# Optimization experiments

Measured on AMD Instinct MI355X. Metric: run time of the kernel, lower is better.

Reference implementation:

```python
import jax, jax.numpy as jnp
import numpy as np
from jax.ops import segment_sum

N_NODES = 100000


def gcn_conv(x, W, b, src, dst, num_nodes):
    # PyG GCNConv: h = x @ W; add self-loops; symmetric normalization; aggregate; + bias
    h = x @ W  # [N, out]
    # add self-loops
    loops = jnp.arange(num_nodes, dtype=src.dtype)
    src_sl = jnp.concatenate([src, loops])
    dst_sl = jnp.concatenate([dst, loops])
    # degree over destination (incl. self-loops), edge weight = 1
    deg = segment_sum(jnp.ones_like(src_sl, dtype=h.dtype), dst_sl, num_segments=num_nodes)
    dinv = jnp.where(deg > 0, jax.lax.rsqrt(deg), 0.0)
    norm = dinv[src_sl] * dinv[dst_sl]  # [E+N]
    msg = h[src_sl] * norm[:, None]      # gather + scale, [E+N, out]
    out = segment_sum(msg, dst_sl, num_segments=num_nodes)  # scatter-add
    return out + b


def setup_inputs() -> dict:
    key = jax.random.key(0)
    ks = jax.random.split(key, 5)
    N, F, C = N_NODES, 64, 10
    E = 1600000
    x = jax.random.normal(ks[0], (N, F), dtype=jnp.float32)
    edge_index = jax.random.randint(ks[1], (2, E), 0, N, dtype=jnp.int64)
    W1 = jax.random.normal(ks[2], (F, 128), dtype=jnp.float32) * (1.0 / np.sqrt(F))
    b1 = jnp.zeros((128,), dtype=jnp.float32)
    W2 = jax.random.normal(ks[3], (128, 16), dtype=jnp.float32) * (1.0 / np.sqrt(128))
    b2 = jnp.zeros((16,), dtype=jnp.float32)
    Wl = jax.random.normal(ks[4], (16, C), dtype=jnp.float32) * (1.0 / np.sqrt(16))
    bl = jnp.zeros((C,), dtype=jnp.float32)
    return {"x": x, "edge_index": edge_index, "W1": W1, "b1": b1,
            "W2": W2, "b2": b2, "Wl": Wl, "bl": bl}


def reference(x, edge_index, W1, b1, W2, b2, Wl, bl):
    src, dst = edge_index[0], edge_index[1]
    h = gcn_conv(x, W1, b1, src, dst, N_NODES)
    h = jax.nn.relu(h)
    h = gcn_conv(h, W2, b2, src, dst, N_NODES)
    h = jax.nn.relu(h)
    return h @ Wl + bl
```

## Files before the change

### kernel.cpp

```cpp
#include <hip/hip_runtime.h>
#include <hip/hip_fp16.h>


#define F_IN 64
#define H1DIM 128
#define H2DIM 16
#define C_OUT 10

#define NBK 1024
#define BSZ_LOG 7
#define BNODES 128
#define CAP 2816
#define SRC_BITS 17

typedef _Float16 f16x8 __attribute__((ext_vector_type(8)));
typedef _Float16 f16x4 __attribute__((ext_vector_type(4)));
typedef float f32x4 __attribute__((ext_vector_type(4)));

__global__ void init_cursors(int* __restrict__ cur) {
    int t = blockIdx.x * 256 + threadIdx.x;
    if (t < NBK) cur[t] = t * CAP;
}

__global__ __launch_bounds__(256) void bucket_scatter(
        const int* __restrict__ ei, int E, int N,
        int* __restrict__ cursor, unsigned* __restrict__ pairs) {
    __shared__ int cnt[NBK];
    __shared__ int base[NBK];
    for (int t = threadIdx.x; t < NBK; t += 256) cnt[t] = 0;
    __syncthreads();

    const int4* s4 = (const int4*)ei;
    const int4* d4 = (const int4*)(ei + E);
    int chunk4 = blockIdx.x * 1024;
    int s_[16], d_[16];
    int m = 0;
#pragma unroll
    for (int r = 0; r < 4; r++) {
        int i4 = chunk4 + r * 256 + threadIdx.x;
        if (i4 * 4 < E) {
            int4 sv = s4[i4], dv = d4[i4];
            int ss[4] = {sv.x, sv.y, sv.z, sv.w};
            int dd[4] = {dv.x, dv.y, dv.z, dv.w};
#pragma unroll
            for (int q = 0; q < 4; q++) {
                if ((unsigned)ss[q] < (unsigned)N && (unsigned)dd[q] < (unsigned)N) {
                    s_[m] = ss[q]; d_[m] = dd[q]; m++;
                }
            }
        }
    }
    for (int k = 0; k < m; k++) atomicAdd(&cnt[d_[k] >> BSZ_LOG], 1);
    __syncthreads();
    for (int t = threadIdx.x; t < NBK; t += 256) {
        int c = cnt[t];
        base[t] = c ? atomicAdd(&cursor[t], c) : 0;
        cnt[t] = 0;
    }
    __syncthreads();
    for (int k = 0; k < m; k++) {
        int b = d_[k] >> BSZ_LOG;
        int pos = base[b] + atomicAdd(&cnt[b], 1);
        if (pos < (b + 1) * CAP)
            pairs[pos] = ((unsigned)(d_[k] & (BNODES - 1)) << SRC_BITS) | (unsigned)s_[k];
    }
}

__global__ __launch_bounds__(256) void build_csr_convert(
        const unsigned* __restrict__ pairs, const int* __restrict__ cursor,
        const float* __restrict__ x, int N,
        float* __restrict__ dinv, int* __restrict__ row_beg,
        int* __restrict__ row_end, int* __restrict__ csr_src,
        __half2* __restrict__ xh2) {
    int b = blockIdx.x;
    int base_node = b << BSZ_LOG;
    int nn = min(BNODES, N - base_node);
    __shared__ int cnt[BNODES];
    __shared__ int sc[BNODES];
    __shared__ int cur[BNODES];
    __shared__ float sdi[BNODES];
    int tid = threadIdx.x;
    if (tid < BNODES) cnt[tid] = 0;
    __syncthreads();

    int pbeg = b * CAP;
    int pend = min(cursor[b], (b + 1) * CAP);
    for (int j = pbeg + tid; j < pend; j += 256)
        atomicAdd(&cnt[pairs[j] >> SRC_BITS], 1);
    __syncthreads();

    int v = (tid < BNODES) ? cnt[tid] : 0;
    if (tid < BNODES) sc[tid] = v;
    __syncthreads();
#pragma unroll
    for (int off = 1; off < BNODES; off <<= 1) {
        int t = (tid < BNODES && tid >= off) ? sc[tid - off] : 0;
        __syncthreads();
        if (tid < BNODES) sc[tid] += t;
        __syncthreads();
    }
    if (tid < nn) {
        int ro = pbeg + sc[tid] - v;
        row_beg[base_node + tid] = ro;
        row_end[base_node + tid] = ro + v;
        cur[tid] = ro;
        float di = rsqrtf((float)(v + 1));
        dinv[base_node + tid] = di;
        sdi[tid] = di;
    }
    __syncthreads();

    for (int j = pbeg + tid; j < pend; j += 256) {
        unsigned p = pairs[j];
        int dl = p >> SRC_BITS, s = p & ((1u << SRC_BITS) - 1);
        int pos = atomicAdd(&cur[dl], 1);
        csr_src[pos] = s;
    }

    const float2* x2 = (const float2*)x;
    int total = nn * 32;
    for (int t = tid; t < total; t += 256) {
        int nl = t >> 5, l = t & 31;
        float di = sdi[nl];
        long long idx = (long long)(base_node + nl) * 32 + l;
        float2 xv = x2[idx];
        xh2[idx] = __floats2half2_rn(xv.x * di, xv.y * di);
    }
}

__global__ __launch_bounds__(256) void gather1_h2(
        const f16x8* __restrict__ xh8, const float* __restrict__ dinv,
        const int* __restrict__ row_beg, const int* __restrict__ row_end,
        const int* __restrict__ csr_src, int N, f16x8* __restrict__ agg1h8) {
    int node = (blockIdx.x * 256 + threadIdx.x) >> 3;
    if (node >= N) return;
    int p = threadIdx.x & 7;
    int beg = row_beg[node], end = row_end[node];
    f16x8 self = xh8[(size_t)node * 8 + p];
    float acc[8];
#pragma unroll
    for (int q = 0; q < 8; q++) acc[q] = (float)self[q];
    int j = beg;
    for (; j + 4 <= end; j += 4) {
        int s0 = csr_src[j], s1 = csr_src[j + 1];
        int s2 = csr_src[j + 2], s3 = csr_src[j + 3];
        f16x8 v0 = xh8[(size_t)s0 * 8 + p];
        f16x8 v1 = xh8[(size_t)s1 * 8 + p];
        f16x8 v2 = xh8[(size_t)s2 * 8 + p];
        f16x8 v3 = xh8[(size_t)s3 * 8 + p];
#pragma unroll
        for (int q = 0; q < 8; q++)
            acc[q] += ((float)v0[q] + (float)v1[q]) + ((float)v2[q] + (float)v3[q]);
    }
    for (; j < end; ++j) {
        f16x8 v = xh8[(size_t)csr_src[j] * 8 + p];
#pragma unroll
        for (int q = 0; q < 8; q++) acc[q] += (float)v[q];
    }
    float di = dinv[node];
    f16x8 o;
#pragma unroll
    for (int q = 0; q < 8; q++) o[q] = (_Float16)(acc[q] * di);
    agg1h8[(size_t)node * 8 + p] = o;
}

__global__ __launch_bounds__(256) void pack_weights(
        const float* __restrict__ W1, const float* __restrict__ W2,
        f16x8* __restrict__ W1p, f16x8* __restrict__ W2p) {
    int s = blockIdx.x * 256 + threadIdx.x;
    if (s < 1024) {
        int frag = s >> 6, lane = s & 63;
        int tile = frag >> 1, kf = frag & 1;
        int c = lane & 15, g = lane >> 4;
        f16x8 v;
#pragma unroll
        for (int j = 0; j < 8; ++j)
            v[j] = (_Float16)W1[(kf * 32 + g * 8 + j) * H1DIM + tile * 16 + c];
        W1p[s] = v;
    } else if (s < 1024 + 256) {
        int s2 = s - 1024;
        int f = s2 >> 6, lane = s2 & 63;
        int c = lane & 15, g = lane >> 4;
        f16x8 v;
#pragma unroll
        for (int j = 0; j < 8; ++j)
            v[j] = (_Float16)W2[(f * 32 + g * 8 + j) * H2DIM + c];
        W2p[s2] = v;
    }
}

__global__ __launch_bounds__(256) void dense1_mfma(
        const _Float16* __restrict__ agg, const f16x8* __restrict__ W1p,
        const f16x8* __restrict__ W2p, const float* __restrict__ b1,
        const float* __restrict__ dinv, int N, _Float16* __restrict__ z2h) {
    __shared__ float sb1[H1DIM];
    __shared__ _Float16 Hl[4][16 * H1DIM];
    if (threadIdx.x < H1DIM) sb1[threadIdx.x] = b1[threadIdx.x];
    __syncthreads();
    const int wave = threadIdx.x >> 6, lane = threadIdx.x & 63;
    const int c = lane & 15, g = lane >> 4;
    const int nodeBase = blockIdx.x * 64 + wave * 16;

    int nld = nodeBase + c; if (nld > N - 1) nld = N - 1;
    const f16x8 a0 = *(const f16x8*)(agg + (size_t)nld * 64 + g * 8);
    const f16x8 a1 = *(const f16x8*)(agg + (size_t)nld * 64 + 32 + g * 8);

    _Float16* hl = Hl[wave];
    const f32x4 zero = {0.f, 0.f, 0.f, 0.f};
#pragma unroll
    for (int t = 0; t < 8; ++t) {
        f32x4 d = __builtin_amdgcn_mfma_f32_16x16x32_f16(W1p[(t * 2 + 1) * 64 + lane], a1, zero, 0, 0, 0);
        d = __builtin_amdgcn_mfma_f32_16x16x32_f16(W1p[(t * 2 + 0) * 64 + lane], a0, d, 0, 0, 0);
        f16x4 hv;
#pragma unroll
        for (int r = 0; r < 4; ++r)
            hv[r] = (_Float16)fmaxf(d[r] + sb1[t * 16 + g * 4 + r], 0.f);
        unsigned byte = ((unsigned)c * 256 + (unsigned)t * 32 + (unsigned)g * 8) ^ ((unsigned)(c & 7) << 4);
        *(f16x4*)((char*)hl + byte) = hv;
    }

    f32x4 acc = zero;
#pragma unroll
    for (int f = 0; f < 4; ++f) {
        unsigned byte = ((unsigned)c * 256 + (unsigned)f * 64 + (unsigned)g * 16) ^ ((unsigned)(c & 7) << 4);
        f16x8 a2 = *(const f16x8*)((char*)hl + byte);
        acc = __builtin_amdgcn_mfma_f32_16x16x32_f16(a2, W2p[f * 64 + lane], acc, 0, 0, 0);
    }
#pragma unroll
    for (int r = 0; r < 4; ++r) {
        int node = nodeBase + g * 4 + r;
        if (node < N) z2h[(size_t)node * 16 + c] = (_Float16)(acc[r] * dinv[node]);
    }
}

__global__ __launch_bounds__(256) void gather2_final_v2(
        const __half2* __restrict__ z2h, const float* __restrict__ dinv,
        const int* __restrict__ row_beg, const int* __restrict__ row_end,
        const int* __restrict__ csr_src,
        const float* __restrict__ b2, const float* __restrict__ Wl,
        const float* __restrict__ bl, int N, float* __restrict__ out) {
    __shared__ float sWl[H2DIM * C_OUT];
    __shared__ float sb2[H2DIM];
    __shared__ float sbl[C_OUT];
    __shared__ float hbuf[32][17];
    int tid = threadIdx.x;
    if (tid < H2DIM * C_OUT) sWl[tid] = Wl[tid];
    if (tid < H2DIM) sb2[tid] = b2[tid];
    if (tid < C_OUT) sbl[tid] = bl[tid];
    __syncthreads();

    int node = blockIdx.x * 32 + (tid >> 3);
    int p = tid & 7;
    int ln = tid >> 3;
    if (node < N) {
        int beg = row_beg[node], end = row_end[node];
        float2 sv = __half22float2(z2h[(size_t)node * 8 + p]);
        float ax = sv.x, ay = sv.y;
        int j = beg;
        for (; j + 4 <= end; j += 4) {
            int s0 = csr_src[j], s1 = csr_src[j + 1];
            int s2 = csr_src[j + 2], s3 = csr_src[j + 3];
            float2 v0 = __half22float2(z2h[(size_t)s0 * 8 + p]);
            float2 v1 = __half22float2(z2h[(size_t)s1 * 8 + p]);
            float2 v2 = __half22float2(z2h[(size_t)s2 * 8 + p]);
            float2 v3 = __half22float2(z2h[(size_t)s3 * 8 + p]);
            ax += (v0.x + v1.x) + (v2.x + v3.x);
            ay += (v0.y + v1.y) + (v2.y + v3.y);
        }
        for (; j < end; ++j) {
            float2 v = __half22float2(z2h[(size_t)csr_src[j] * 8 + p]);
            ax += v.x; ay += v.y;
        }
        float di = dinv[node];
        hbuf[ln][2 * p]     = fmaxf(ax * di + sb2[2 * p], 0.f);
        hbuf[ln][2 * p + 1] = fmaxf(ay * di + sb2[2 * p + 1], 0.f);
    }
    __syncthreads();
    if (node < N) {
        float o0 = sbl[p];
        float o1 = (p < 2) ? sbl[8 + p] : 0.f;
#pragma unroll
        for (int k = 0; k < H2DIM; k++) {
            float hk = hbuf[ln][k];
            o0 = fmaf(hk, sWl[k * C_OUT + p], o0);
            if (p < 2) o1 = fmaf(hk, sWl[k * C_OUT + 8 + p], o1);
        }
        out[(size_t)node * C_OUT + p] = o0;
        if (p < 2) out[(size_t)node * C_OUT + 8 + p] = o1;
    }
}

extern "C" void kernel_launch(void* const* d_in, const int* in_sizes, int n_in,
                              void* d_out, int out_size, void* d_ws, size_t ws_size,
                              hipStream_t stream) {
    const float* x  = (const float*)d_in[0];
    const int*   ei = (const int*)d_in[1];
    const float* W1 = (const float*)d_in[2];
    const float* b1 = (const float*)d_in[3];
    const float* W2 = (const float*)d_in[4];
    const float* b2 = (const float*)d_in[5];
    const float* Wl = (const float*)d_in[6];
    const float* bl = (const float*)d_in[7];
    float* out = (float*)d_out;

    const int N = in_sizes[0] / F_IN;
    const int E = in_sizes[1] / 2;

    size_t off = 0;
    auto carve = [&](size_t bytes) {
        void* p = (char*)d_ws + off;
        off += (bytes + 255) & ~(size_t)255;
        return p;
    };
    float*   dinv    = (float*)  carve((size_t)N * sizeof(float));
    int*     row_beg = (int*)    carve((size_t)N * sizeof(int));
    int*     row_end = (int*)    carve((size_t)N * sizeof(int));
    int*     csr_src = (int*)    carve((size_t)NBK * CAP * sizeof(int));
    __half2* xh2     = (__half2*)carve((size_t)N * 32 * sizeof(__half2));
    size_t agg_bytes = (size_t)N * 32 * sizeof(__half2);
    size_t pr_bytes  = (size_t)NBK * CAP * sizeof(unsigned);
    __half2* agg1h   = (__half2*)carve(agg_bytes > pr_bytes ? agg_bytes : pr_bytes);
    __half2* z2h     = (__half2*)carve((size_t)N * 8 * sizeof(__half2));
    int*     bcur    = (int*)    carve(NBK * sizeof(int));
    f16x8*   W1p     = (f16x8*)  carve(1024 * sizeof(f16x8));
    f16x8*   W2p     = (f16x8*)  carve(256 * sizeof(f16x8));
    unsigned* pairs = (unsigned*)agg1h;

    const int nbuckets_used = (N + BNODES - 1) >> BSZ_LOG;

    init_cursors<<<(NBK + 255) / 256, 256, 0, stream>>>(bcur);
    pack_weights<<<5, 256, 0, stream>>>(W1, W2, W1p, W2p);
    bucket_scatter<<<(E + 4095) / 4096, 256, 0, stream>>>(ei, E, N, bcur, pairs);
    build_csr_convert<<<nbuckets_used, 256, 0, stream>>>(
        pairs, bcur, x, N, dinv, row_beg, row_end, csr_src, xh2);

    gather1_h2<<<((size_t)N * 8 + 255) / 256, 256, 0, stream>>>(
        (const f16x8*)xh2, dinv, row_beg, row_end, csr_src, N, (f16x8*)agg1h);
    dense1_mfma<<<(N + 63) / 64, 256, 0, stream>>>(
        (const _Float16*)agg1h, W1p, W2p, b1, dinv, N, (_Float16*)z2h);
    gather2_final_v2<<<(N + 31) / 32, 256, 0, stream>>>(
        z2h, dinv, row_beg, row_end, csr_src, b2, Wl, bl, N, out);
}
```

Measured before the change: 114.4 us.

## Merge setup kernels, stage bucket pairs in LDS, unroll gathers by eight

Merges cursor initialization and weight packing into one setup kernel, removing a launch. The CSR build kernel now copies each bucket's pairs into shared memory once and reuses them for both the counting and placement passes, instead of reading global memory twice. Both gather kernels gain an 8-way unrolled edge loop to put more independent loads in flight. This raises register and LDS use (about 11 KB per block for the pairs buffer), which may reduce occupancy.

Result: faster. 111.4 us (-2.6%).

```diff
diff --git a/kernel.cpp b/kernel.cpp
--- a/kernel.cpp
+++ b/kernel.cpp
@@ -17,9 +17,33 @@
 typedef _Float16 f16x4 __attribute__((ext_vector_type(4)));
 typedef float f32x4 __attribute__((ext_vector_type(4)));
 
-__global__ void init_cursors(int* __restrict__ cur) {
-    int t = blockIdx.x * 256 + threadIdx.x;
-    if (t < NBK) cur[t] = t * CAP;
+__global__ __launch_bounds__(256) void setup_kernel(
+        const float* __restrict__ W1, const float* __restrict__ W2,
+        f16x8* __restrict__ W1p, f16x8* __restrict__ W2p,
+        int* __restrict__ cur) {
+    int s = blockIdx.x * 256 + threadIdx.x;
+    if (s < 1024) {
+        int frag = s >> 6, lane = s & 63;
+        int tile = frag >> 1, kf = frag & 1;
+        int c = lane & 15, g = lane >> 4;
+        f16x8 v;
+#pragma unroll
+        for (int j = 0; j < 8; ++j)
+            v[j] = (_Float16)W1[(kf * 32 + g * 8 + j) * H1DIM + tile * 16 + c];
+        W1p[s] = v;
+    } else if (s < 1024 + 256) {
+        int s2 = s - 1024;
+        int f = s2 >> 6, lane = s2 & 63;
+        int c = lane & 15, g = lane >> 4;
+        f16x8 v;
+#pragma unroll
+        for (int j = 0; j < 8; ++j)
+            v[j] = (_Float16)W2[(f * 32 + g * 8 + j) * H2DIM + c];
+        W2p[s2] = v;
+    } else {
+        int t = s - 1280;
+        if (t >= 0 && t < NBK) cur[t] = t * CAP;
+    }
 }
 
 __global__ __launch_bounds__(256) void bucket_scatter(
@@ -75,18 +99,22 @@
     int b = blockIdx.x;
     int base_node = b << BSZ_LOG;
     int nn = min(BNODES, N - base_node);
+    __shared__ unsigned lp[CAP];
     __shared__ int cnt[BNODES];
     __shared__ int sc[BNODES];
     __shared__ int cur[BNODES];
     __shared__ float sdi[BNODES];
     int tid = threadIdx.x;
     if (tid < BNODES) cnt[tid] = 0;
-    __syncthreads();
 
     int pbeg = b * CAP;
     int pend = min(cursor[b], (b + 1) * CAP);
-    for (int j = pbeg + tid; j < pend; j += 256)
-        atomicAdd(&cnt[pairs[j] >> SRC_BITS], 1);
+    int np = pend - pbeg;
+    for (int j = tid; j < np; j += 256) lp[j] = pairs[pbeg + j];
+    __syncthreads();
+
+    for (int j = tid; j < np; j += 256)
+        atomicAdd(&cnt[lp[j] >> SRC_BITS], 1);
     __syncthreads();
 
     int v = (tid < BNODES) ? cnt[tid] : 0;
@@ -110,8 +138,8 @@
     }
     __syncthreads();
 
-    for (int j = pbeg + tid; j < pend; j += 256) {
-        unsigned p = pairs[j];
+    for (int j = tid; j < np; j += 256) {
+        unsigned p = lp[j];
         int dl = p >> SRC_BITS, s = p & ((1u << SRC_BITS) - 1);
         int pos = atomicAdd(&cur[dl], 1);
         csr_src[pos] = s;
@@ -141,6 +169,24 @@
 #pragma unroll
     for (int q = 0; q < 8; q++) acc[q] = (float)self[q];
     int j = beg;
+    for (; j + 8 <= end; j += 8) {
+        int s0 = csr_src[j],     s1 = csr_src[j + 1];
+        int s2 = csr_src[j + 2], s3 = csr_src[j + 3];
+        int s4 = csr_src[j + 4], s5 = csr_src[j + 5];
+        int s6 = csr_src[j + 6], s7 = csr_src[j + 7];
+        f16x8 v0 = xh8[(size_t)s0 * 8 + p];
+        f16x8 v1 = xh8[(size_t)s1 * 8 + p];
+        f16x8 v2 = xh8[(size_t)s2 * 8 + p];
+        f16x8 v3 = xh8[(size_t)s3 * 8 + p];
+        f16x8 v4 = xh8[(size_t)s4 * 8 + p];
+        f16x8 v5 = xh8[(size_t)s5 * 8 + p];
+        f16x8 v6 = xh8[(size_t)s6 * 8 + p];
+        f16x8 v7 = xh8[(size_t)s7 * 8 + p];
+#pragma unroll
+        for (int q = 0; q < 8; q++)
+            acc[q] += (((float)v0[q] + (float)v1[q]) + ((float)v2[q] + (float)v3[q]))
+                    + (((float)v4[q] + (float)v5[q]) + ((float)v6[q] + (float)v7[q]));
+    }
     for (; j + 4 <= end; j += 4) {
         int s0 = csr_src[j], s1 = csr_src[j + 1];
         int s2 = csr_src[j + 2], s3 = csr_src[j + 3];
@@ -162,31 +208,6 @@
 #pragma unroll
     for (int q = 0; q < 8; q++) o[q] = (_Float16)(acc[q] * di);
     agg1h8[(size_t)node * 8 + p] = o;
-}
-
-__global__ __launch_bounds__(256) void pack_weights(
-        const float* __restrict__ W1, const float* __restrict__ W2,
-        f16x8* __restrict__ W1p, f16x8* __restrict__ W2p) {
-    int s = blockIdx.x * 256 + threadIdx.x;
-    if (s < 1024) {
-        int frag = s >> 6, lane = s & 63;
-        int tile = frag >> 1, kf = frag & 1;
-        int c = lane & 15, g = lane >> 4;
-        f16x8 v;
-#pragma unroll
-        for (int j = 0; j < 8; ++j)
-            v[j] = (_Float16)W1[(kf * 32 + g * 8 + j) * H1DIM + tile * 16 + c];
-        W1p[s] = v;
-    } else if (s < 1024 + 256) {
-        int s2 = s - 1024;
-        int f = s2 >> 6, lane = s2 & 63;
-        int c = lane & 15, g = lane >> 4;
-        f16x8 v;
-#pragma unroll
-        for (int j = 0; j < 8; ++j)
-            v[j] = (_Float16)W2[(f * 32 + g * 8 + j) * H2DIM + c];
-        W2p[s2] = v;
-    }
 }
 
 __global__ __launch_bounds__(256) void dense1_mfma(
@@ -257,6 +278,22 @@
         float2 sv = __half22float2(z2h[(size_t)node * 8 + p]);
         float ax = sv.x, ay = sv.y;
         int j = beg;
+        for (; j + 8 <= end; j += 8) {
+            int s0 = csr_src[j],     s1 = csr_src[j + 1];
+            int s2 = csr_src[j + 2], s3 = csr_src[j + 3];
+            int s4 = csr_src[j + 4], s5 = csr_src[j + 5];
+            int s6 = csr_src[j + 6], s7 = csr_src[j + 7];
+            float2 v0 = __half22float2(z2h[(size_t)s0 * 8 + p]);
+            float2 v1 = __half22float2(z2h[(size_t)s1 * 8 + p]);
+            float2 v2 = __half22float2(z2h[(size_t)s2 * 8 + p]);
+            float2 v3 = __half22float2(z2h[(size_t)s3 * 8 + p]);
+            float2 v4 = __half22float2(z2h[(size_t)s4 * 8 + p]);
+            float2 v5 = __half22float2(z2h[(size_t)s5 * 8 + p]);
+            float2 v6 = __half22float2(z2h[(size_t)s6 * 8 + p]);
+            float2 v7 = __half22float2(z2h[(size_t)s7 * 8 + p]);
+            ax += ((v0.x + v1.x) + (v2.x + v3.x)) + ((v4.x + v5.x) + (v6.x + v7.x));
+            ay += ((v0.y + v1.y) + (v2.y + v3.y)) + ((v4.y + v5.y) + (v6.y + v7.y));
+        }
         for (; j + 4 <= end; j += 4) {
             int s0 = csr_src[j], s1 = csr_src[j + 1];
             int s2 = csr_src[j + 2], s3 = csr_src[j + 3];
@@ -328,8 +365,7 @@
 
     const int nbuckets_used = (N + BNODES - 1) >> BSZ_LOG;
 
-    init_cursors<<<(NBK + 255) / 256, 256, 0, stream>>>(bcur);
-    pack_weights<<<5, 256, 0, stream>>>(W1, W2, W1p, W2p);
+    setup_kernel<<<10, 256, 0, stream>>>(W1, W2, W1p, W2p, bcur);
     bucket_scatter<<<(E + 4095) / 4096, 256, 0, stream>>>(ei, E, N, bcur, pairs);
     build_csr_convert<<<nbuckets_used, 256, 0, stream>>>(
         pairs, bcur, x, N, dinv, row_beg, row_end, csr_src, xh2);
```
